# Kernel tuning notes

Hardware: AMD Instinct MI355X
Metric: run time of the kernel (lower is better)

The kernel has to match this reference:

```python
import jax, jax.numpy as jnp
import numpy as np

DIM = 256
NUM_EXPERTS = 16
EXPERT_HIDDEN = 128
ROUTER_HIDDEN = 64
N_TOKENS = 32768


def setup_inputs() -> dict:
    key = jax.random.key(0)
    ks = jax.random.split(key, 9)
    s = lambda fan_in: 1.0 / np.sqrt(fan_in)
    x = jax.random.normal(ks[0], (N_TOKENS, DIM), dtype=jnp.float32)
    # Router params (Linear(DIM,64) -> ReLU -> Linear(64,E))
    r_w1 = jax.random.uniform(ks[1], (DIM, ROUTER_HIDDEN), jnp.float32, -s(DIM), s(DIM))
    r_b1 = jax.random.uniform(ks[2], (ROUTER_HIDDEN,), jnp.float32, -s(DIM), s(DIM))
    r_w2 = jax.random.uniform(ks[3], (ROUTER_HIDDEN, NUM_EXPERTS), jnp.float32, -s(ROUTER_HIDDEN), s(ROUTER_HIDDEN))
    r_b2 = jax.random.uniform(ks[4], (NUM_EXPERTS,), jnp.float32, -s(ROUTER_HIDDEN), s(ROUTER_HIDDEN))
    # Expert params, stacked over experts: Linear(DIM,128) -> Tanh -> Linear(128,DIM)
    e_w1 = jax.random.uniform(ks[5], (NUM_EXPERTS, DIM, EXPERT_HIDDEN), jnp.float32, -s(DIM), s(DIM))
    e_b1 = jax.random.uniform(ks[6], (NUM_EXPERTS, EXPERT_HIDDEN), jnp.float32, -s(DIM), s(DIM))
    e_w2 = jax.random.uniform(ks[7], (NUM_EXPERTS, EXPERT_HIDDEN, DIM), jnp.float32, -s(EXPERT_HIDDEN), s(EXPERT_HIDDEN))
    e_b2 = jax.random.uniform(ks[8], (NUM_EXPERTS, DIM), jnp.float32, -s(EXPERT_HIDDEN), s(EXPERT_HIDDEN))
    return {"x": x, "r_w1": r_w1, "r_b1": r_b1, "r_w2": r_w2, "r_b2": r_b2,
            "e_w1": e_w1, "e_b1": e_b1, "e_w2": e_w2, "e_b2": e_b2}


def reference(x, r_w1, r_b1, r_w2, r_b2, e_w1, e_b1, e_w2, e_b2):
    # Router: softmax(Linear(ReLU(Linear(x)))), temp=1.0
    h_r = jax.nn.relu(x @ r_w1 + r_b1)                      # [N, 64]
    w = jax.nn.softmax(h_r @ r_w2 + r_b2, axis=-1)          # [N, E]
    # All experts densely (faithful to the reference loop), batched over E.
    h = jnp.tanh(jnp.einsum('nd,edh->neh', x, e_w1) + e_b1[None, :, :])   # [N, E, H]
    outs = jnp.einsum('neh,ehd->ned', h, e_w2) + e_b2[None, :, :]         # [N, E, D]
    # Top-2 gating: mask, renormalize, combine.
    top_val, top_idx = jax.lax.top_k(w, 2)                  # [N, 2]
    n = w.shape[0]
    mask = jnp.zeros_like(w).at[jnp.arange(n)[:, None], top_idx].set(1.0)
    w_top = w * mask
    w_top = w_top / (jnp.sum(w_top, axis=-1, keepdims=True) + 1e-8)
    y_pred = jnp.einsum('ne,ned->nd', w_top, outs)          # [N, D]
    return (y_pred, w)
```

## Files before the change

kernel.cpp:

```cpp
#include <hip/hip_runtime.h>
#include <math.h>

#define NT 32768
#define DIM 256
#define NE 16
#define EH 128
#define RH 64
#define TB 64

#define IB (NT * DIM)
#define WS_COUNTS (IB)
#define WS_OFFSETS (IB + 16)
#define WS_CURSORS (IB + 33)
#define WS_NBLK (IB + 49)
#define WS_TABLE (IB + 64)
#define WS_TOKE (IB + 4096)
#define WS_LIST (WS_TOKE + 2 * NT)
#define WS_TOKG (WS_LIST + 2 * NT)
#define WS_LIST_G (WS_TOKG + 2 * NT)
#define WS_END_I (WS_LIST_G + 2 * NT)
#define U_W1T (2 * WS_END_I)
#define U_W2T (U_W1T + NE * DIM * EH)

typedef __attribute__((ext_vector_type(4))) float f32x4;
typedef __attribute__((ext_vector_type(8))) short bf16x8;
typedef __attribute__((ext_vector_type(8))) unsigned short us8;

#define SWZ9(b) ((b) ^ (((b) >> 5) & 0x70))
#define SWZ8(b) ((b) ^ (((b) >> 4) & 0x70))

__device__ inline unsigned short f2bf(float f) {
    unsigned int bits = __builtin_bit_cast(unsigned int, f);
    bits += 0x7fffu + ((bits >> 16) & 1u);
    return (unsigned short)(bits >> 16);
}

__global__ __launch_bounds__(256) void router_kernel(
    const float* __restrict__ x,
    const float* __restrict__ rw1, const float* __restrict__ rb1,
    const float* __restrict__ rw2, const float* __restrict__ rb2,
    float* __restrict__ w_out, int* __restrict__ wsi, float* __restrict__ wsf)
{
    __shared__ float xT[64][68];
    __shared__ float w1s[64][64];
    __shared__ float hs[64][68];
    __shared__ float ls[64][20];
    __shared__ int scnt[16];

    const int tid = threadIdx.x;
    const int tok0 = blockIdx.x * 64;
    if (tid < 16) scnt[tid] = 0;

    float acc[4][4];
#pragma unroll
    for (int i = 0; i < 4; ++i)
#pragma unroll
        for (int j = 0; j < 4; ++j) acc[i][j] = 0.f;

    const int tt = (tid & 15) * 4;
    const int hh = (tid >> 4) * 4;

    for (int kc = 0; kc < 4; ++kc) {
        __syncthreads();
#pragma unroll
        for (int i = 0; i < 4; ++i) {
            int idx = tid + 256 * i;
            int t = idx >> 4;
            int d4 = (idx & 15) * 4;
            float4 v = *(const float4*)(x + (size_t)(tok0 + t) * DIM + kc * 64 + d4);
            xT[d4 + 0][t] = v.x; xT[d4 + 1][t] = v.y;
            xT[d4 + 2][t] = v.z; xT[d4 + 3][t] = v.w;
        }
#pragma unroll
        for (int i = 0; i < 4; ++i) {
            int idx = tid + 256 * i;
            int d = idx >> 4;
            int h4 = (idx & 15) * 4;
            *(float4*)&w1s[d][h4] = *(const float4*)(rw1 + (size_t)(kc * 64 + d) * RH + h4);
        }
        __syncthreads();
#pragma unroll 8
        for (int d = 0; d < 64; ++d) {
            const float4 xa4 = *(const float4*)&xT[d][tt];
            const float4 wv4 = *(const float4*)&w1s[d][hh];
            const float xa[4] = {xa4.x, xa4.y, xa4.z, xa4.w};
            const float wv[4] = {wv4.x, wv4.y, wv4.z, wv4.w};
#pragma unroll
            for (int i = 0; i < 4; ++i)
#pragma unroll
                for (int j = 0; j < 4; ++j)
                    acc[i][j] = fmaf(xa[i], wv[j], acc[i][j]);
        }
    }
    __syncthreads();
    {
        const float4 b4 = *(const float4*)(rb1 + hh);
        const float b[4] = {b4.x, b4.y, b4.z, b4.w};
#pragma unroll
        for (int i = 0; i < 4; ++i) {
            float4 hv;
            hv.x = fmaxf(acc[i][0] + b[0], 0.f);
            hv.y = fmaxf(acc[i][1] + b[1], 0.f);
            hv.z = fmaxf(acc[i][2] + b[2], 0.f);
            hv.w = fmaxf(acc[i][3] + b[3], 0.f);
            *(float4*)&hs[tt + i][hh] = hv;
        }
    }
    __syncthreads();
    {
        int tok = tid >> 2;
        int e0 = (tid & 3) * 4;
        float l[4] = {0.f, 0.f, 0.f, 0.f};
#pragma unroll 8
        for (int k = 0; k < 64; ++k) {
            float hv = hs[tok][k];
            float4 wv = *(const float4*)(rw2 + k * NE + e0);
            l[0] = fmaf(hv, wv.x, l[0]);
            l[1] = fmaf(hv, wv.y, l[1]);
            l[2] = fmaf(hv, wv.z, l[2]);
            l[3] = fmaf(hv, wv.w, l[3]);
        }
        float4 lb = *(const float4*)(rb2 + e0);
        ls[tok][e0 + 0] = l[0] + lb.x;
        ls[tok][e0 + 1] = l[1] + lb.y;
        ls[tok][e0 + 2] = l[2] + lb.z;
        ls[tok][e0 + 3] = l[3] + lb.w;
    }
    __syncthreads();
    if (tid < 64) {
        const int tok = tid;
        const int gt = tok0 + tok;
        float v[16];
        float m = -1e30f;
#pragma unroll
        for (int e = 0; e < 16; ++e) { v[e] = ls[tok][e]; m = fmaxf(m, v[e]); }
        float s = 0.f;
#pragma unroll
        for (int e = 0; e < 16; ++e) { v[e] = expf(v[e] - m); s += v[e]; }
        const float inv = 1.0f / s;
#pragma unroll
        for (int e = 0; e < 16; ++e) v[e] *= inv;
#pragma unroll
        for (int e = 0; e < 16; e += 4) {
            float4 wv = make_float4(v[e], v[e + 1], v[e + 2], v[e + 3]);
            *(float4*)(w_out + (size_t)gt * NE + e) = wv;
        }
        float v1 = -1.f, v2 = -1.f; int i1 = 0, i2 = 0;
#pragma unroll
        for (int e = 0; e < 16; ++e) {
            if (v[e] > v1) { v2 = v1; i2 = i1; v1 = v[e]; i1 = e; }
            else if (v[e] > v2) { v2 = v[e]; i2 = e; }
        }
        const float den = v1 + v2 + 1e-8f;
        atomicAdd(&scnt[i1], 1);
        atomicAdd(&scnt[i2], 1);
        wsi[WS_TOKE + 2 * gt + 0] = i1;
        wsi[WS_TOKE + 2 * gt + 1] = i2;
        wsf[WS_TOKG + 2 * gt + 0] = v1 / den;
        wsf[WS_TOKG + 2 * gt + 1] = v2 / den;
    }
    __syncthreads();
    if (tid < 16 && scnt[tid]) atomicAdd(&wsi[WS_COUNTS + tid], scnt[tid]);
}

__global__ __launch_bounds__(256) void wprep_kernel(
    const float* __restrict__ ew1, const float* __restrict__ ew2,
    unsigned short* __restrict__ w1t, unsigned short* __restrict__ w2t)
{
    __shared__ float t[64][65];
    int b = blockIdx.x;
    const float* src; unsigned short* dst; int R, C, tr, tc;
    if (b < 128) {
        int e = b >> 3, t8 = b & 7; tr = t8 >> 1; tc = t8 & 1;
        src = ew1 + (size_t)e * DIM * EH; R = DIM; C = EH;
        dst = w1t + (size_t)e * DIM * EH;
    } else {
        int b2 = b - 128; int e = b2 >> 3, t8 = b2 & 7; tr = t8 & 1; tc = t8 >> 1;
        src = ew2 + (size_t)e * EH * DIM; R = EH; C = DIM;
        dst = w2t + (size_t)e * EH * DIM;
    }
    const int R0 = tr * 64, C0 = tc * 64;
    const int tid = threadIdx.x;
#pragma unroll
    for (int q = 0; q < 4; ++q) {
        int r = (tid >> 4) + q * 16, c = (tid & 15) * 4;
        float4 v = *(const float4*)(src + (size_t)(R0 + r) * C + C0 + c);
        t[r][c] = v.x; t[r][c + 1] = v.y; t[r][c + 2] = v.z; t[r][c + 3] = v.w;
    }
    __syncthreads();
#pragma unroll
    for (int q = 0; q < 2; ++q) {
        int rp = (tid >> 3) + q * 32, c0 = (tid & 7) * 8;
        us8 u;
#pragma unroll
        for (int k = 0; k < 8; ++k) u[k] = f2bf(t[c0 + k][rp]);
        *(us8*)(dst + (size_t)(C0 + rp) * R + R0 + c0) = u;
    }
}

__global__ __launch_bounds__(64) void scan_kernel(int* __restrict__ wsi)
{
    __shared__ int soff[17], snc[16];
    const int tid = threadIdx.x;
    if (tid == 0) {
        int off = 0, nb = 0;
        soff[0] = 0;
        for (int e = 0; e < NE; ++e) {
            int c = wsi[WS_COUNTS + e];
            wsi[WS_CURSORS + e] = off;
            wsi[WS_OFFSETS + e] = off;
            off += c;
            soff[e + 1] = off;
            snc[e] = nb;
            nb += (c + TB - 1) / TB;
        }
        wsi[WS_OFFSETS + NE] = off;
        wsi[WS_NBLK] = nb;
    }
    __syncthreads();
    for (int e = 0; e < NE; ++e) {
        int nc = (soff[e + 1] - soff[e] + TB - 1) / TB;
        for (int k = tid; k < nc; k += 64)
            wsi[WS_TABLE + snc[e] + k] = (e << 16) | k;
    }
}

__global__ __launch_bounds__(256) void scatter_kernel(int* __restrict__ wsi, float* __restrict__ wsf)
{
    __shared__ int scnt[16], sbase[16];
    const int tid = threadIdx.x;
    const int t = blockIdx.x * 256 + tid;
    if (tid < 16) scnt[tid] = 0;
    __syncthreads();
    const int e0 = wsi[WS_TOKE + 2 * t + 0];
    const int e1 = wsi[WS_TOKE + 2 * t + 1];
    const int l0 = atomicAdd(&scnt[e0], 1);
    const int l1 = atomicAdd(&scnt[e1], 1);
    __syncthreads();
    if (tid < 16) sbase[tid] = scnt[tid] ? atomicAdd(&wsi[WS_CURSORS + tid], scnt[tid]) : 0;
    __syncthreads();
    const int p0 = sbase[e0] + l0;
    const int p1 = sbase[e1] + l1;
    wsi[WS_LIST + p0] = (t << 1);
    wsf[WS_LIST_G + p0] = wsf[WS_TOKG + 2 * t + 0];
    wsi[WS_LIST + p1] = (t << 1) | 1;
    wsf[WS_LIST_G + p1] = wsf[WS_TOKG + 2 * t + 1];
}

__global__ __launch_bounds__(256, 4) void expert_kernel(
    const float* __restrict__ x,
    const float* __restrict__ eb1, const float* __restrict__ eb2,
    const unsigned short* __restrict__ w1t, const unsigned short* __restrict__ w2t,
    const int* __restrict__ wsi, const float* __restrict__ wsf,
    float* __restrict__ y, float* __restrict__ part1)
{
    __shared__ unsigned short smem[16384];
    if ((int)blockIdx.x >= wsi[WS_NBLK]) return;

    const int ent = wsi[WS_TABLE + blockIdx.x];
    const int e = ent >> 16;
    const int c = ent & 0xffff;
    const int start = wsi[WS_OFFSETS + e] + c * TB;
    const int cnt = min(TB, wsi[WS_OFFSETS + e + 1] - start);

    const int tid = threadIdx.x;
    const int lane = tid & 63, w = tid >> 6;
    const int l15 = lane & 15;
    const int kq = lane >> 4;
    const int q4 = kq * 4;
    char* lds = (char*)smem;

    const char* w1e = (const char*)(w1t + (size_t)e * DIM * EH);
    bf16x8 b1[8][2];
#pragma unroll
    for (int ks = 0; ks < 8; ++ks)
#pragma unroll
        for (int nt = 0; nt < 2; ++nt)
            b1[ks][nt] = *(const bf16x8*)(w1e + (w * 32 + nt * 16 + l15) * 512 + ks * 64 + kq * 16);

    {
        const int row = tid >> 2, q = tid & 3;
        const int srow = (row < cnt) ? (wsi[WS_LIST + start + row] >> 1) : -1;
        const float* xr = x + (size_t)(srow < 0 ? 0 : srow) * DIM + q * 64;
        const int base = row * 512 + q * 128;
#pragma unroll
        for (int i = 0; i < 8; ++i) {
            us8 u;
            if (srow >= 0) {
                float4 a = *(const float4*)(xr + i * 8);
                float4 b = *(const float4*)(xr + i * 8 + 4);
                u[0] = f2bf(a.x); u[1] = f2bf(a.y); u[2] = f2bf(a.z); u[3] = f2bf(a.w);
                u[4] = f2bf(b.x); u[5] = f2bf(b.y); u[6] = f2bf(b.z); u[7] = f2bf(b.w);
            } else {
#pragma unroll
                for (int k = 0; k < 8; ++k) u[k] = 0;
            }
            *(us8*)(lds + SWZ9(base + i * 16)) = u;
        }
    }
    __syncthreads();

    f32x4 zero4; zero4[0] = zero4[1] = zero4[2] = zero4[3] = 0.f;
    f32x4 acc[4][2];
#pragma unroll
    for (int i = 0; i < 4; ++i)
#pragma unroll
        for (int j = 0; j < 2; ++j) acc[i][j] = zero4;

#pragma unroll
    for (int ks = 0; ks < 8; ++ks) {
        bf16x8 a[4];
#pragma unroll
        for (int mt = 0; mt < 4; ++mt)
            a[mt] = *(const bf16x8*)(lds + SWZ9((mt * 16 + l15) * 512 + ks * 64 + kq * 16));
#pragma unroll
        for (int mt = 0; mt < 4; ++mt)
#pragma unroll
            for (int nt = 0; nt < 2; ++nt)
                acc[mt][nt] = __builtin_amdgcn_mfma_f32_16x16x32_bf16(a[mt], b1[ks][nt], acc[mt][nt], 0, 0, 0);
    }

    const char* w2e = (const char*)(w2t + (size_t)e * EH * DIM);
    bf16x8 b2a[4][2];
#pragma unroll
    for (int ks = 0; ks < 4; ++ks)
#pragma unroll
        for (int nt = 0; nt < 2; ++nt)
            b2a[ks][nt] = *(const bf16x8*)(w2e + (w * 64 + nt * 16 + l15) * 256 + ks * 64 + kq * 16);

    __syncthreads();

#pragma unroll
    for (int nt = 0; nt < 2; ++nt) {
        const int h = w * 32 + nt * 16 + l15;
        const float b1v = eb1[e * EH + h];
#pragma unroll
        for (int mt = 0; mt < 4; ++mt)
#pragma unroll
            for (int r = 0; r < 4; ++r) {
                int tok = mt * 16 + q4 + r;
                *(unsigned short*)(lds + SWZ8(tok * 256 + h * 2)) = f2bf(tanhf(acc[mt][nt][r] + b1v));
            }
    }
    __syncthreads();

    bf16x8 b2b[4][2];
#pragma unroll
    for (int ks = 0; ks < 4; ++ks)
#pragma unroll
        for (int nt = 0; nt < 2; ++nt)
            b2b[ks][nt] = *(const bf16x8*)(w2e + (w * 64 + 32 + nt * 16 + l15) * 256 + ks * 64 + kq * 16);

#pragma unroll
    for (int half = 0; half < 2; ++half) {
        auto& bsel = half ? b2b : b2a;
        f32x4 acc2[4][2];
#pragma unroll
        for (int i = 0; i < 4; ++i)
#pragma unroll
            for (int j = 0; j < 2; ++j) acc2[i][j] = zero4;
#pragma unroll
        for (int ks = 0; ks < 4; ++ks) {
            bf16x8 a[4];
#pragma unroll
            for (int mt = 0; mt < 4; ++mt)
                a[mt] = *(const bf16x8*)(lds + SWZ8((mt * 16 + l15) * 256 + ks * 64 + kq * 16));
#pragma unroll
            for (int mt = 0; mt < 4; ++mt)
#pragma unroll
                for (int nt = 0; nt < 2; ++nt)
                    acc2[mt][nt] = __builtin_amdgcn_mfma_f32_16x16x32_bf16(a[mt], bsel[ks][nt], acc2[mt][nt], 0, 0, 0);
        }
        float b2v[2];
#pragma unroll
        for (int nt = 0; nt < 2; ++nt)
            b2v[nt] = eb2[e * DIM + w * 64 + half * 32 + nt * 16 + l15];
#pragma unroll
        for (int mt = 0; mt < 4; ++mt)
#pragma unroll
            for (int r = 0; r < 4; ++r) {
                int rl = mt * 16 + q4 + r;
                if (rl < cnt) {
                    int entry = wsi[WS_LIST + start + rl];
                    int tok = entry >> 1;
                    float g = wsf[WS_LIST_G + start + rl];
                    float* dst = ((entry & 1) ? part1 : y) + (size_t)tok * DIM + w * 64 + half * 32;
#pragma unroll
                    for (int nt = 0; nt < 2; ++nt)
                        dst[nt * 16 + l15] = g * (acc2[mt][nt][r] + b2v[nt]);
                }
            }
    }
}

__global__ __launch_bounds__(256) void combine_kernel(float* __restrict__ y,
                                                      const float* __restrict__ part1)
{
    const size_t i = ((size_t)blockIdx.x * 256 + threadIdx.x) * 4;
    float4 a = *(float4*)(y + i);
    const float4 b = *(const float4*)(part1 + i);
    a.x += b.x; a.y += b.y; a.z += b.z; a.w += b.w;
    *(float4*)(y + i) = a;
}

extern "C" void kernel_launch(void* const* d_in, const int* in_sizes, int n_in,
                              void* d_out, int out_size, void* d_ws, size_t ws_size,
                              hipStream_t stream)
{
    const float* x = (const float*)d_in[0];
    const float* rw1 = (const float*)d_in[1];
    const float* rb1 = (const float*)d_in[2];
    const float* rw2 = (const float*)d_in[3];
    const float* rb2 = (const float*)d_in[4];
    const float* ew1 = (const float*)d_in[5];
    const float* eb1 = (const float*)d_in[6];
    const float* ew2 = (const float*)d_in[7];
    const float* eb2 = (const float*)d_in[8];

    float* y = (float*)d_out;
    float* w_out = y + (size_t)NT * DIM;
    int* wsi = (int*)d_ws;
    float* wsf = (float*)d_ws;
    float* part1 = (float*)d_ws;
    unsigned short* wsu = (unsigned short*)d_ws;

    hipMemsetAsync(wsi + WS_COUNTS, 0, NE * sizeof(int), stream);

    wprep_kernel<<<256, 256, 0, stream>>>(ew1, ew2, wsu + U_W1T, wsu + U_W2T);
    router_kernel<<<NT / 64, 256, 0, stream>>>(x, rw1, rb1, rw2, rb2, w_out, wsi, wsf);
    scan_kernel<<<1, 64, 0, stream>>>(wsi);
    scatter_kernel<<<NT / 256, 256, 0, stream>>>(wsi, wsf);
    expert_kernel<<<2 * NT / TB + NE, 256, 0, stream>>>(x, eb1, eb2, wsu + U_W1T, wsu + U_W2T,
                                                        wsi, wsf, y, part1);
    combine_kernel<<<NT * DIM / 1024, 256, 0, stream>>>(y, part1);
}
```

Before: 137.8 us.

## Fuse router and dense all-expert compute into a single per-tile kernel

Replaces the routed pipeline (router, scan, scatter, per-expert blocks, combine) with one kernel that computes router softmax/top-2 gates into LDS, then loops over all 16 experts densely per 64-token tile, accumulating gated outputs in registers. This removes several launches, global atomics, index lists and the partial-sum combine pass. It trades these for 8x the expert FLOPs and low occupancy (one large-LDS block per CU), and uses a fast exp-based tanh.

```diff
diff --git a/kernel.cpp b/kernel.cpp
--- a/kernel.cpp
+++ b/kernel.cpp
@@ -6,20 +6,8 @@
 #define NE 16
 #define EH 128
 #define RH 64
-#define TB 64
-
-#define IB (NT * DIM)
-#define WS_COUNTS (IB)
-#define WS_OFFSETS (IB + 16)
-#define WS_CURSORS (IB + 33)
-#define WS_NBLK (IB + 49)
-#define WS_TABLE (IB + 64)
-#define WS_TOKE (IB + 4096)
-#define WS_LIST (WS_TOKE + 2 * NT)
-#define WS_TOKG (WS_LIST + 2 * NT)
-#define WS_LIST_G (WS_TOKG + 2 * NT)
-#define WS_END_I (WS_LIST_G + 2 * NT)
-#define U_W1T (2 * WS_END_I)
+
+#define U_W1T 0
 #define U_W2T (U_W1T + NE * DIM * EH)
 
 typedef __attribute__((ext_vector_type(4))) float f32x4;
@@ -34,133 +22,10 @@
     bits += 0x7fffu + ((bits >> 16) & 1u);
     return (unsigned short)(bits >> 16);
 }
-
-__global__ __launch_bounds__(256) void router_kernel(
-    const float* __restrict__ x,
-    const float* __restrict__ rw1, const float* __restrict__ rb1,
-    const float* __restrict__ rw2, const float* __restrict__ rb2,
-    float* __restrict__ w_out, int* __restrict__ wsi, float* __restrict__ wsf)
-{
-    __shared__ float xT[64][68];
-    __shared__ float w1s[64][64];
-    __shared__ float hs[64][68];
-    __shared__ float ls[64][20];
-    __shared__ int scnt[16];
-
-    const int tid = threadIdx.x;
-    const int tok0 = blockIdx.x * 64;
-    if (tid < 16) scnt[tid] = 0;
-
-    float acc[4][4];
-#pragma unroll
-    for (int i = 0; i < 4; ++i)
-#pragma unroll
-        for (int j = 0; j < 4; ++j) acc[i][j] = 0.f;
-
-    const int tt = (tid & 15) * 4;
-    const int hh = (tid >> 4) * 4;
-
-    for (int kc = 0; kc < 4; ++kc) {
-        __syncthreads();
-#pragma unroll
-        for (int i = 0; i < 4; ++i) {
-            int idx = tid + 256 * i;
-            int t = idx >> 4;
-            int d4 = (idx & 15) * 4;
-            float4 v = *(const float4*)(x + (size_t)(tok0 + t) * DIM + kc * 64 + d4);
-            xT[d4 + 0][t] = v.x; xT[d4 + 1][t] = v.y;
-            xT[d4 + 2][t] = v.z; xT[d4 + 3][t] = v.w;
-        }
-#pragma unroll
-        for (int i = 0; i < 4; ++i) {
-            int idx = tid + 256 * i;
-            int d = idx >> 4;
-            int h4 = (idx & 15) * 4;
-            *(float4*)&w1s[d][h4] = *(const float4*)(rw1 + (size_t)(kc * 64 + d) * RH + h4);
-        }
-        __syncthreads();
-#pragma unroll 8
-        for (int d = 0; d < 64; ++d) {
-            const float4 xa4 = *(const float4*)&xT[d][tt];
-            const float4 wv4 = *(const float4*)&w1s[d][hh];
-            const float xa[4] = {xa4.x, xa4.y, xa4.z, xa4.w};
-            const float wv[4] = {wv4.x, wv4.y, wv4.z, wv4.w};
-#pragma unroll
-            for (int i = 0; i < 4; ++i)
-#pragma unroll
-                for (int j = 0; j < 4; ++j)
-                    acc[i][j] = fmaf(xa[i], wv[j], acc[i][j]);
-        }
-    }
-    __syncthreads();
-    {
-        const float4 b4 = *(const float4*)(rb1 + hh);
-        const float b[4] = {b4.x, b4.y, b4.z, b4.w};
-#pragma unroll
-        for (int i = 0; i < 4; ++i) {
-            float4 hv;
-            hv.x = fmaxf(acc[i][0] + b[0], 0.f);
-            hv.y = fmaxf(acc[i][1] + b[1], 0.f);
-            hv.z = fmaxf(acc[i][2] + b[2], 0.f);
-            hv.w = fmaxf(acc[i][3] + b[3], 0.f);
-            *(float4*)&hs[tt + i][hh] = hv;
-        }
-    }
-    __syncthreads();
-    {
-        int tok = tid >> 2;
-        int e0 = (tid & 3) * 4;
-        float l[4] = {0.f, 0.f, 0.f, 0.f};
-#pragma unroll 8
-        for (int k = 0; k < 64; ++k) {
-            float hv = hs[tok][k];
-            float4 wv = *(const float4*)(rw2 + k * NE + e0);
-            l[0] = fmaf(hv, wv.x, l[0]);
-            l[1] = fmaf(hv, wv.y, l[1]);
-            l[2] = fmaf(hv, wv.z, l[2]);
-            l[3] = fmaf(hv, wv.w, l[3]);
-        }
-        float4 lb = *(const float4*)(rb2 + e0);
-        ls[tok][e0 + 0] = l[0] + lb.x;
-        ls[tok][e0 + 1] = l[1] + lb.y;
-        ls[tok][e0 + 2] = l[2] + lb.z;
-        ls[tok][e0 + 3] = l[3] + lb.w;
-    }
-    __syncthreads();
-    if (tid < 64) {
-        const int tok = tid;
-        const int gt = tok0 + tok;
-        float v[16];
-        float m = -1e30f;
-#pragma unroll
-        for (int e = 0; e < 16; ++e) { v[e] = ls[tok][e]; m = fmaxf(m, v[e]); }
-        float s = 0.f;
-#pragma unroll
-        for (int e = 0; e < 16; ++e) { v[e] = expf(v[e] - m); s += v[e]; }
-        const float inv = 1.0f / s;
-#pragma unroll
-        for (int e = 0; e < 16; ++e) v[e] *= inv;
-#pragma unroll
-        for (int e = 0; e < 16; e += 4) {
-            float4 wv = make_float4(v[e], v[e + 1], v[e + 2], v[e + 3]);
-            *(float4*)(w_out + (size_t)gt * NE + e) = wv;
-        }
-        float v1 = -1.f, v2 = -1.f; int i1 = 0, i2 = 0;
-#pragma unroll
-        for (int e = 0; e < 16; ++e) {
-            if (v[e] > v1) { v2 = v1; i2 = i1; v1 = v[e]; i1 = e; }
-            else if (v[e] > v2) { v2 = v[e]; i2 = e; }
-        }
-        const float den = v1 + v2 + 1e-8f;
-        atomicAdd(&scnt[i1], 1);
-        atomicAdd(&scnt[i2], 1);
-        wsi[WS_TOKE + 2 * gt + 0] = i1;
-        wsi[WS_TOKE + 2 * gt + 1] = i2;
-        wsf[WS_TOKG + 2 * gt + 0] = v1 / den;
-        wsf[WS_TOKG + 2 * gt + 1] = v2 / den;
-    }
-    __syncthreads();
-    if (tid < 16 && scnt[tid]) atomicAdd(&wsi[WS_COUNTS + tid], scnt[tid]);
+__device__ inline float fast_tanh(float v) {
+    float cv = fminf(fmaxf(v, -15.f), 15.f);
+    float ex = __expf(2.f * cv);
+    return (ex - 1.f) / (ex + 1.f);
 }
 
 __global__ __launch_bounds__(256) void wprep_kernel(
@@ -198,209 +63,259 @@
     }
 }
 
-__global__ __launch_bounds__(64) void scan_kernel(int* __restrict__ wsi)
-{
-    __shared__ int soff[17], snc[16];
-    const int tid = threadIdx.x;
-    if (tid == 0) {
-        int off = 0, nb = 0;
-        soff[0] = 0;
-        for (int e = 0; e < NE; ++e) {
-            int c = wsi[WS_COUNTS + e];
-            wsi[WS_CURSORS + e] = off;
-            wsi[WS_OFFSETS + e] = off;
-            off += c;
-            soff[e + 1] = off;
-            snc[e] = nb;
-            nb += (c + TB - 1) / TB;
-        }
-        wsi[WS_OFFSETS + NE] = off;
-        wsi[WS_NBLK] = nb;
-    }
-    __syncthreads();
-    for (int e = 0; e < NE; ++e) {
-        int nc = (soff[e + 1] - soff[e] + TB - 1) / TB;
-        for (int k = tid; k < nc; k += 64)
-            wsi[WS_TABLE + snc[e] + k] = (e << 16) | k;
-    }
-}
-
-__global__ __launch_bounds__(256) void scatter_kernel(int* __restrict__ wsi, float* __restrict__ wsf)
-{
-    __shared__ int scnt[16], sbase[16];
-    const int tid = threadIdx.x;
-    const int t = blockIdx.x * 256 + tid;
-    if (tid < 16) scnt[tid] = 0;
-    __syncthreads();
-    const int e0 = wsi[WS_TOKE + 2 * t + 0];
-    const int e1 = wsi[WS_TOKE + 2 * t + 1];
-    const int l0 = atomicAdd(&scnt[e0], 1);
-    const int l1 = atomicAdd(&scnt[e1], 1);
-    __syncthreads();
-    if (tid < 16) sbase[tid] = scnt[tid] ? atomicAdd(&wsi[WS_CURSORS + tid], scnt[tid]) : 0;
-    __syncthreads();
-    const int p0 = sbase[e0] + l0;
-    const int p1 = sbase[e1] + l1;
-    wsi[WS_LIST + p0] = (t << 1);
-    wsf[WS_LIST_G + p0] = wsf[WS_TOKG + 2 * t + 0];
-    wsi[WS_LIST + p1] = (t << 1) | 1;
-    wsf[WS_LIST_G + p1] = wsf[WS_TOKG + 2 * t + 1];
-}
-
-__global__ __launch_bounds__(256, 4) void expert_kernel(
+__global__ __launch_bounds__(256, 1) void mega_kernel(
     const float* __restrict__ x,
+    const float* __restrict__ rw1, const float* __restrict__ rb1,
+    const float* __restrict__ rw2, const float* __restrict__ rb2,
     const float* __restrict__ eb1, const float* __restrict__ eb2,
     const unsigned short* __restrict__ w1t, const unsigned short* __restrict__ w2t,
-    const int* __restrict__ wsi, const float* __restrict__ wsf,
-    float* __restrict__ y, float* __restrict__ part1)
+    float* __restrict__ w_out, float* __restrict__ y)
 {
-    __shared__ unsigned short smem[16384];
-    if ((int)blockIdx.x >= wsi[WS_NBLK]) return;
-
-    const int ent = wsi[WS_TABLE + blockIdx.x];
-    const int e = ent >> 16;
-    const int c = ent & 0xffff;
-    const int start = wsi[WS_OFFSETS + e] + c * TB;
-    const int cnt = min(TB, wsi[WS_OFFSETS + e + 1] - start);
-
+    __shared__ char pool[69632];
     const int tid = threadIdx.x;
+    const int tok0 = blockIdx.x * 64;
+
+    float (*xT)[68]  = (float(*)[68])pool;
+    float (*w1s)[64] = (float(*)[64])(pool + 17408);
+    float (*hs)[68]  = (float(*)[68])(pool + 33792);
+    float (*ls)[20]  = (float(*)[20])(pool + 51200);
+    float* g_lds     = (float*)(pool + 65536);
+
+    {
+        float acc[4][4];
+#pragma unroll
+        for (int i = 0; i < 4; ++i)
+#pragma unroll
+            for (int j = 0; j < 4; ++j) acc[i][j] = 0.f;
+
+        const int tt = (tid & 15) * 4;
+        const int hh = (tid >> 4) * 4;
+
+        for (int kc = 0; kc < 4; ++kc) {
+            __syncthreads();
+#pragma unroll
+            for (int i = 0; i < 4; ++i) {
+                int idx = tid + 256 * i;
+                int t2 = idx >> 4;
+                int d4 = (idx & 15) * 4;
+                float4 v = *(const float4*)(x + (size_t)(tok0 + t2) * DIM + kc * 64 + d4);
+                xT[d4 + 0][t2] = v.x; xT[d4 + 1][t2] = v.y;
+                xT[d4 + 2][t2] = v.z; xT[d4 + 3][t2] = v.w;
+            }
+#pragma unroll
+            for (int i = 0; i < 4; ++i) {
+                int idx = tid + 256 * i;
+                int d = idx >> 4;
+                int h4 = (idx & 15) * 4;
+                *(float4*)&w1s[d][h4] = *(const float4*)(rw1 + (size_t)(kc * 64 + d) * RH + h4);
+            }
+            __syncthreads();
+#pragma unroll 8
+            for (int d = 0; d < 64; ++d) {
+                const float4 xa4 = *(const float4*)&xT[d][tt];
+                const float4 wv4 = *(const float4*)&w1s[d][hh];
+                const float xa[4] = {xa4.x, xa4.y, xa4.z, xa4.w};
+                const float wv[4] = {wv4.x, wv4.y, wv4.z, wv4.w};
+#pragma unroll
+                for (int i = 0; i < 4; ++i)
+#pragma unroll
+                    for (int j = 0; j < 4; ++j)
+                        acc[i][j] = fmaf(xa[i], wv[j], acc[i][j]);
+            }
+        }
+        __syncthreads();
+        {
+            const float4 b4 = *(const float4*)(rb1 + hh);
+            const float b[4] = {b4.x, b4.y, b4.z, b4.w};
+#pragma unroll
+            for (int i = 0; i < 4; ++i) {
+                float4 hv;
+                hv.x = fmaxf(acc[i][0] + b[0], 0.f);
+                hv.y = fmaxf(acc[i][1] + b[1], 0.f);
+                hv.z = fmaxf(acc[i][2] + b[2], 0.f);
+                hv.w = fmaxf(acc[i][3] + b[3], 0.f);
+                *(float4*)&hs[tt + i][hh] = hv;
+            }
+        }
+        __syncthreads();
+        {
+            int tok = tid >> 2;
+            int e0 = (tid & 3) * 4;
+            float l[4] = {0.f, 0.f, 0.f, 0.f};
+#pragma unroll 8
+            for (int k = 0; k < 64; ++k) {
+                float hv = hs[tok][k];
+                float4 wv = *(const float4*)(rw2 + k * NE + e0);
+                l[0] = fmaf(hv, wv.x, l[0]);
+                l[1] = fmaf(hv, wv.y, l[1]);
+                l[2] = fmaf(hv, wv.z, l[2]);
+                l[3] = fmaf(hv, wv.w, l[3]);
+            }
+            float4 lb = *(const float4*)(rb2 + e0);
+            ls[tok][e0 + 0] = l[0] + lb.x;
+            ls[tok][e0 + 1] = l[1] + lb.y;
+            ls[tok][e0 + 2] = l[2] + lb.z;
+            ls[tok][e0 + 3] = l[3] + lb.w;
+        }
+        __syncthreads();
+        if (tid < 64) {
+            const int tok = tid;
+            const int gt = tok0 + tok;
+            float v[16];
+            float m = -1e30f;
+#pragma unroll
+            for (int e = 0; e < 16; ++e) { v[e] = ls[tok][e]; m = fmaxf(m, v[e]); }
+            float s = 0.f;
+#pragma unroll
+            for (int e = 0; e < 16; ++e) { v[e] = expf(v[e] - m); s += v[e]; }
+            const float inv = 1.0f / s;
+#pragma unroll
+            for (int e = 0; e < 16; ++e) v[e] *= inv;
+#pragma unroll
+            for (int e = 0; e < 16; e += 4) {
+                float4 wv = make_float4(v[e], v[e + 1], v[e + 2], v[e + 3]);
+                *(float4*)(w_out + (size_t)gt * NE + e) = wv;
+            }
+            float v1 = -1.f, v2 = -1.f; int i1 = 0, i2 = 0;
+#pragma unroll
+            for (int e = 0; e < 16; ++e) {
+                if (v[e] > v1) { v2 = v1; i2 = i1; v1 = v[e]; i1 = e; }
+                else if (v[e] > v2) { v2 = v[e]; i2 = e; }
+            }
+            const float den = v1 + v2 + 1e-8f;
+#pragma unroll
+            for (int e = 0; e < 16; ++e) g_lds[tok * 16 + e] = 0.f;
+            g_lds[tok * 16 + i1] = v1 / den;
+            g_lds[tok * 16 + i2] = v2 / den;
+        }
+        __syncthreads();
+    }
+
+    {
+        const int row = tid >> 2, q = tid & 3;
+        const float* xr = x + (size_t)(tok0 + row) * DIM + q * 64;
+        const int base = row * 512 + q * 128;
+#pragma unroll
+        for (int i = 0; i < 8; ++i) {
+            float4 a = *(const float4*)(xr + i * 8);
+            float4 b = *(const float4*)(xr + i * 8 + 4);
+            us8 u;
+            u[0] = f2bf(a.x); u[1] = f2bf(a.y); u[2] = f2bf(a.z); u[3] = f2bf(a.w);
+            u[4] = f2bf(b.x); u[5] = f2bf(b.y); u[6] = f2bf(b.z); u[7] = f2bf(b.w);
+            *(us8*)(pool + SWZ9(base + i * 16)) = u;
+        }
+    }
+    __syncthreads();
+
     const int lane = tid & 63, w = tid >> 6;
     const int l15 = lane & 15;
     const int kq = lane >> 4;
     const int q4 = kq * 4;
-    char* lds = (char*)smem;
-
-    const char* w1e = (const char*)(w1t + (size_t)e * DIM * EH);
-    bf16x8 b1[8][2];
-#pragma unroll
-    for (int ks = 0; ks < 8; ++ks)
-#pragma unroll
-        for (int nt = 0; nt < 2; ++nt)
-            b1[ks][nt] = *(const bf16x8*)(w1e + (w * 32 + nt * 16 + l15) * 512 + ks * 64 + kq * 16);
-
+    f32x4 zero4; zero4[0] = zero4[1] = zero4[2] = zero4[3] = 0.f;
+
+    f32x4 y_acc[4][4];
+#pragma unroll
+    for (int i = 0; i < 4; ++i)
+#pragma unroll
+        for (int j = 0; j < 4; ++j) y_acc[i][j] = zero4;
+
+#pragma unroll 1
+    for (int e = 0; e < NE; ++e) {
+        const char* w1e = (const char*)(w1t + (size_t)e * DIM * EH);
+        bf16x8 b1[8][2];
+#pragma unroll
+        for (int ks = 0; ks < 8; ++ks)
+#pragma unroll
+            for (int nt = 0; nt < 2; ++nt)
+                b1[ks][nt] = *(const bf16x8*)(w1e + (w * 32 + nt * 16 + l15) * 512 + ks * 64 + kq * 16);
+
+        f32x4 acc1[4][2];
+#pragma unroll
+        for (int i = 0; i < 4; ++i)
+#pragma unroll
+            for (int j = 0; j < 2; ++j) acc1[i][j] = zero4;
+
+#pragma unroll
+        for (int ks = 0; ks < 8; ++ks) {
+            bf16x8 a[4];
+#pragma unroll
+            for (int mt = 0; mt < 4; ++mt)
+                a[mt] = *(const bf16x8*)(pool + SWZ9((mt * 16 + l15) * 512 + ks * 64 + kq * 16));
+#pragma unroll
+            for (int mt = 0; mt < 4; ++mt)
+#pragma unroll
+                for (int nt = 0; nt < 2; ++nt)
+                    acc1[mt][nt] = __builtin_amdgcn_mfma_f32_16x16x32_bf16(a[mt], b1[ks][nt], acc1[mt][nt], 0, 0, 0);
+        }
+
+        char* hTb = pool + 32768 + (e & 1) * 16384;
+#pragma unroll
+        for (int nt = 0; nt < 2; ++nt) {
+            const int h = w * 32 + nt * 16 + l15;
+            const float b1v = eb1[e * EH + h];
+#pragma unroll
+            for (int mt = 0; mt < 4; ++mt)
+#pragma unroll
+                for (int r = 0; r < 4; ++r) {
+                    int tok = mt * 16 + q4 + r;
+                    *(unsigned short*)(hTb + SWZ8(tok * 256 + h * 2)) = f2bf(fast_tanh(acc1[mt][nt][r] + b1v));
+                }
+        }
+        __syncthreads();
+
+        const char* w2e = (const char*)(w2t + (size_t)e * EH * DIM);
+        bf16x8 b2[4][4];
+#pragma unroll
+        for (int nt = 0; nt < 4; ++nt)
+#pragma unroll
+            for (int ks = 0; ks < 4; ++ks)
+                b2[nt][ks] = *(const bf16x8*)(w2e + (w * 64 + nt * 16 + l15) * 256 + ks * 64 + kq * 16);
+        float b2v[4];
+#pragma unroll
+        for (int nt = 0; nt < 4; ++nt)
+            b2v[nt] = eb2[e * DIM + w * 64 + nt * 16 + l15];
+
+#pragma unroll
+        for (int mt = 0; mt < 4; ++mt) {
+            bf16x8 a2[4];
+#pragma unroll
+            for (int ks = 0; ks < 4; ++ks)
+                a2[ks] = *(const bf16x8*)(hTb + SWZ8((mt * 16 + l15) * 256 + ks * 64 + kq * 16));
+            float g4[4];
+#pragma unroll
+            for (int r = 0; r < 4; ++r)
+                g4[r] = g_lds[(mt * 16 + q4 + r) * 16 + e];
+#pragma unroll
+            for (int nt = 0; nt < 4; ++nt) {
+                f32x4 acc2 = zero4;
+#pragma unroll
+                for (int ks = 0; ks < 4; ++ks)
+                    acc2 = __builtin_amdgcn_mfma_f32_16x16x32_bf16(a2[ks], b2[nt][ks], acc2, 0, 0, 0);
+#pragma unroll
+                for (int r = 0; r < 4; ++r)
+                    y_acc[mt][nt][r] = fmaf(g4[r], acc2[r] + b2v[nt], y_acc[mt][nt][r]);
+            }
+        }
+    }
+
+    __syncthreads();
+    float* obufF = (float*)pool;
+#pragma unroll
+    for (int mt = 0; mt < 4; ++mt)
+#pragma unroll
+        for (int nt = 0; nt < 4; ++nt)
+#pragma unroll
+            for (int r = 0; r < 4; ++r)
+                obufF[(mt * 16 + q4 + r) * 260 + w * 64 + nt * 16 + l15] = y_acc[mt][nt][r];
+    __syncthreads();
     {
-        const int row = tid >> 2, q = tid & 3;
-        const int srow = (row < cnt) ? (wsi[WS_LIST + start + row] >> 1) : -1;
-        const float* xr = x + (size_t)(srow < 0 ? 0 : srow) * DIM + q * 64;
-        const int base = row * 512 + q * 128;
-#pragma unroll
-        for (int i = 0; i < 8; ++i) {
-            us8 u;
-            if (srow >= 0) {
-                float4 a = *(const float4*)(xr + i * 8);
-                float4 b = *(const float4*)(xr + i * 8 + 4);
-                u[0] = f2bf(a.x); u[1] = f2bf(a.y); u[2] = f2bf(a.z); u[3] = f2bf(a.w);
-                u[4] = f2bf(b.x); u[5] = f2bf(b.y); u[6] = f2bf(b.z); u[7] = f2bf(b.w);
-            } else {
-#pragma unroll
-                for (int k = 0; k < 8; ++k) u[k] = 0;
-            }
-            *(us8*)(lds + SWZ9(base + i * 16)) = u;
-        }
-    }
-    __syncthreads();
-
-    f32x4 zero4; zero4[0] = zero4[1] = zero4[2] = zero4[3] = 0.f;
-    f32x4 acc[4][2];
-#pragma unroll
-    for (int i = 0; i < 4; ++i)
-#pragma unroll
-        for (int j = 0; j < 2; ++j) acc[i][j] = zero4;
-
-#pragma unroll
-    for (int ks = 0; ks < 8; ++ks) {
-        bf16x8 a[4];
-#pragma unroll
-        for (int mt = 0; mt < 4; ++mt)
-            a[mt] = *(const bf16x8*)(lds + SWZ9((mt * 16 + l15) * 512 + ks * 64 + kq * 16));
-#pragma unroll
-        for (int mt = 0; mt < 4; ++mt)
-#pragma unroll
-            for (int nt = 0; nt < 2; ++nt)
-                acc[mt][nt] = __builtin_amdgcn_mfma_f32_16x16x32_bf16(a[mt], b1[ks][nt], acc[mt][nt], 0, 0, 0);
-    }
-
-    const char* w2e = (const char*)(w2t + (size_t)e * EH * DIM);
-    bf16x8 b2a[4][2];
-#pragma unroll
-    for (int ks = 0; ks < 4; ++ks)
-#pragma unroll
-        for (int nt = 0; nt < 2; ++nt)
-            b2a[ks][nt] = *(const bf16x8*)(w2e + (w * 64 + nt * 16 + l15) * 256 + ks * 64 + kq * 16);
-
-    __syncthreads();
-
-#pragma unroll
-    for (int nt = 0; nt < 2; ++nt) {
-        const int h = w * 32 + nt * 16 + l15;
-        const float b1v = eb1[e * EH + h];
-#pragma unroll
-        for (int mt = 0; mt < 4; ++mt)
-#pragma unroll
-            for (int r = 0; r < 4; ++r) {
-                int tok = mt * 16 + q4 + r;
-                *(unsigned short*)(lds + SWZ8(tok * 256 + h * 2)) = f2bf(tanhf(acc[mt][nt][r] + b1v));
-            }
-    }
-    __syncthreads();
-
-    bf16x8 b2b[4][2];
-#pragma unroll
-    for (int ks = 0; ks < 4; ++ks)
-#pragma unroll
-        for (int nt = 0; nt < 2; ++nt)
-            b2b[ks][nt] = *(const bf16x8*)(w2e + (w * 64 + 32 + nt * 16 + l15) * 256 + ks * 64 + kq * 16);
-
-#pragma unroll
-    for (int half = 0; half < 2; ++half) {
-        auto& bsel = half ? b2b : b2a;
-        f32x4 acc2[4][2];
-#pragma unroll
-        for (int i = 0; i < 4; ++i)
-#pragma unroll
-            for (int j = 0; j < 2; ++j) acc2[i][j] = zero4;
-#pragma unroll
-        for (int ks = 0; ks < 4; ++ks) {
-            bf16x8 a[4];
-#pragma unroll
-            for (int mt = 0; mt < 4; ++mt)
-                a[mt] = *(const bf16x8*)(lds + SWZ8((mt * 16 + l15) * 256 + ks * 64 + kq * 16));
-#pragma unroll
-            for (int mt = 0; mt < 4; ++mt)
-#pragma unroll
-                for (int nt = 0; nt < 2; ++nt)
-                    acc2[mt][nt] = __builtin_amdgcn_mfma_f32_16x16x32_bf16(a[mt], bsel[ks][nt], acc2[mt][nt], 0, 0, 0);
-        }
-        float b2v[2];
-#pragma unroll
-        for (int nt = 0; nt < 2; ++nt)
-            b2v[nt] = eb2[e * DIM + w * 64 + half * 32 + nt * 16 + l15];
-#pragma unroll
-        for (int mt = 0; mt < 4; ++mt)
-#pragma unroll
-            for (int r = 0; r < 4; ++r) {
-                int rl = mt * 16 + q4 + r;
-                if (rl < cnt) {
-                    int entry = wsi[WS_LIST + start + rl];
-                    int tok = entry >> 1;
-                    float g = wsf[WS_LIST_G + start + rl];
-                    float* dst = ((entry & 1) ? part1 : y) + (size_t)tok * DIM + w * 64 + half * 32;
-#pragma unroll
-                    for (int nt = 0; nt < 2; ++nt)
-                        dst[nt * 16 + l15] = g * (acc2[mt][nt][r] + b2v[nt]);
-                }
-            }
-    }
-}
-
-__global__ __launch_bounds__(256) void combine_kernel(float* __restrict__ y,
-                                                      const float* __restrict__ part1)
-{
-    const size_t i = ((size_t)blockIdx.x * 256 + threadIdx.x) * 4;
-    float4 a = *(float4*)(y + i);
-    const float4 b = *(const float4*)(part1 + i);
-    a.x += b.x; a.y += b.y; a.z += b.z; a.w += b.w;
-    *(float4*)(y + i) = a;
+        const int row = tid >> 2, qd = tid & 3;
+        float* dst = y + (size_t)(tok0 + row) * DIM + qd * 64;
+        const float* srcl = obufF + row * 260 + qd * 64;
+#pragma unroll
+        for (int i = 0; i < 16; ++i)
+            *(float4*)(dst + i * 4) = *(const float4*)(srcl + i * 4);
+    }
 }
 
 extern "C" void kernel_launch(void* const* d_in, const int* in_sizes, int n_in,
@@ -419,18 +334,9 @@
 
     float* y = (float*)d_out;
     float* w_out = y + (size_t)NT * DIM;
-    int* wsi = (int*)d_ws;
-    float* wsf = (float*)d_ws;
-    float* part1 = (float*)d_ws;
     unsigned short* wsu = (unsigned short*)d_ws;
 
-    hipMemsetAsync(wsi + WS_COUNTS, 0, NE * sizeof(int), stream);
-
     wprep_kernel<<<256, 256, 0, stream>>>(ew1, ew2, wsu + U_W1T, wsu + U_W2T);
-    router_kernel<<<NT / 64, 256, 0, stream>>>(x, rw1, rb1, rw2, rb2, w_out, wsi, wsf);
-    scan_kernel<<<1, 64, 0, stream>>>(wsi);
-    scatter_kernel<<<NT / 256, 256, 0, stream>>>(wsi, wsf);
-    expert_kernel<<<2 * NT / TB + NE, 256, 0, stream>>>(x, eb1, eb2, wsu + U_W1T, wsu + U_W2T,
-                                                        wsi, wsf, y, part1);
-    combine_kernel<<<NT * DIM / 1024, 256, 0, stream>>>(y, part1);
-}
+    mega_kernel<<<NT / 64, 256, 0, stream>>>(x, rw1, rb1, rw2, rb2, eb1, eb2,
+                                             wsu + U_W1T, wsu + U_W2T, w_out, y);
+}
```

Measured after the change: 280.0 us. +103.2%, slower.
